# Kernel tuning notes

Measured on AMD Instinct MI355X. Metric: run time of the kernel, lower is better.

Reference implementation:

```python
import jax, jax.numpy as jnp
import numpy as np

B, S, D = 4, 2048, 256
H, RANK, DFF = 8, 8, 1024
DK = D // H
EPS = 1e-5


def _linear(x, W, b):
    # torch nn.Linear: y = x @ W.T + b, W shape (out, in)
    return jnp.einsum('bsd,od->bso', x, W) + b


def _layer_norm(x, g, b):
    mu = jnp.mean(x, axis=-1, keepdims=True)
    var = jnp.var(x, axis=-1, keepdims=True)
    return (x - mu) * jax.lax.rsqrt(var + EPS) * g + b


def setup_inputs() -> dict:
    key = jax.random.key(0)
    ks = jax.random.split(key, 20)
    r = RANK * H
    s = lambda fan_in: 1.0 / np.sqrt(fan_in)
    inp = {
        'x': jax.random.normal(ks[0], (B, S, D), jnp.float32),
        'Wq_down': jax.random.uniform(ks[1], (r, D), jnp.float32, -s(D), s(D)),
        'bq_down': jnp.zeros((r,), jnp.float32),
        'Wq_up': jax.random.uniform(ks[2], (D, r), jnp.float32, -s(r), s(r)),
        'bq_up': jnp.zeros((D,), jnp.float32),
        'Wk_down': jax.random.uniform(ks[3], (r, D), jnp.float32, -s(D), s(D)),
        'bk_down': jnp.zeros((r,), jnp.float32),
        'Wk_up': jax.random.uniform(ks[4], (D, r), jnp.float32, -s(r), s(r)),
        'bk_up': jnp.zeros((D,), jnp.float32),
        'Wv': jax.random.uniform(ks[5], (D, D), jnp.float32, -s(D), s(D)),
        'bv': jnp.zeros((D,), jnp.float32),
        'Wo': jax.random.uniform(ks[6], (D, D), jnp.float32, -s(D), s(D)),
        'bo': jnp.zeros((D,), jnp.float32),
        'ln_attn_g': jnp.ones((D,), jnp.float32),
        'ln_attn_b': jnp.zeros((D,), jnp.float32),
        'W_ff1': jax.random.uniform(ks[7], (DFF, D), jnp.float32, -s(D), s(D)),
        'b_ff1': jnp.zeros((DFF,), jnp.float32),
        'W_ff2': jax.random.uniform(ks[8], (D, DFF), jnp.float32, -s(DFF), s(DFF)),
        'b_ff2': jnp.zeros((D,), jnp.float32),
        'ln_blk_g': jnp.ones((D,), jnp.float32),
        'ln_blk_b': jnp.zeros((D,), jnp.float32),
    }
    return inp


def reference(x, Wq_down, bq_down, Wq_up, bq_up, Wk_down, bk_down, Wk_up, bk_up,
              Wv, bv, Wo, bo, ln_attn_g, ln_attn_b,
              W_ff1, b_ff1, W_ff2, b_ff2, ln_blk_g, ln_blk_b):
    # Low-rank Q/K: down-project to rank*H then up-project to D
    Q = _linear(_linear(x, Wq_down, bq_down), Wq_up, bq_up)
    K = _linear(_linear(x, Wk_down, bk_down), Wk_up, bk_up)
    V = _linear(x, Wv, bv)
    # (B,S,D) -> (B,H,S,DK)
    Q = Q.reshape(B, S, H, DK).transpose(0, 2, 1, 3)
    K = K.reshape(B, S, H, DK).transpose(0, 2, 1, 3)
    V = V.reshape(B, S, H, DK).transpose(0, 2, 1, 3)
    scale = 1.0 / np.sqrt(DK).astype(np.float32)
    scores = jnp.einsum('bhqd,bhkd->bhqk', Q, K) * scale
    attn = jax.nn.softmax(scores, axis=-1)
    context = jnp.einsum('bhqk,bhkd->bhqd', attn, V)
    context = context.transpose(0, 2, 1, 3).reshape(B, S, D)
    attn_out = _linear(context, Wo, bo)
    attn_out = _layer_norm(x + attn_out, ln_attn_g, ln_attn_b)
    # FFN: Linear -> GELU (exact erf, torch default) -> Linear
    h = jax.nn.gelu(_linear(attn_out, W_ff1, b_ff1), approximate=False)
    ff = _linear(h, W_ff2, b_ff2)
    return _layer_norm(attn_out + ff, ln_blk_g, ln_blk_b)
```

## Files before the change

### kernel.cpp

```cpp
#include <hip/hip_runtime.h>
#include <hip/hip_bf16.h>
#include <math.h>

#define NB 4
#define NS 2048
#define ND 256
#define NH 8
#define NDK 32
#define NDFF 1024
#define NROWS (NB * NS)
#define KC 4
#define KVB 64
#define KTILES (NS / KC / KVB)
#define QVLD 384

using short8 = __attribute__((ext_vector_type(8))) short;
using f32x4  = __attribute__((ext_vector_type(4))) float;

__device__ __forceinline__ unsigned short f2bf(float f) {
  union { float f; unsigned u; } v; v.f = f;
  unsigned r = v.u + 0x7fffu + ((v.u >> 16) & 1u);
  return (unsigned short)(r >> 16);
}
__device__ __forceinline__ float bf2f(unsigned short u) {
  union { unsigned u; float f; } v; v.u = ((unsigned)u) << 16;
  return v.f;
}
__device__ __forceinline__ unsigned cvt_pk_bf16(float lo, float hi) {
  unsigned r;
  asm("v_cvt_pk_bf16_f32 %0, %1, %2" : "=v"(r) : "v"(lo), "v"(hi));
  return r;
}
__device__ __forceinline__ void gl_lds16(const void* g, void* l) {
  __builtin_amdgcn_global_load_lds(
      (const __attribute__((address_space(1))) unsigned int*)g,
      (__attribute__((address_space(3))) unsigned int*)l, 16, 0, 0);
}

__global__ void cvt_batch(const float* s0, const float* s1, const float* s2,
                          const float* s3, const float* s4, const float* s5,
                          const float* s6, const float* s7, const float* s8,
                          unsigned short* d0, unsigned short* d1,
                          unsigned short* d2, unsigned short* d3,
                          unsigned short* d4, unsigned short* d5,
                          unsigned short* d6, unsigned short* d7,
                          unsigned short* d8,
                          int n0, int n1, int n2, int n3, int n4, int n5,
                          int n6, int n7, int n8) {
  const float* s; unsigned short* d; int n;
  switch (blockIdx.y) {
    case 0: s = s0; d = d0; n = n0; break;
    case 1: s = s1; d = d1; n = n1; break;
    case 2: s = s2; d = d2; n = n2; break;
    case 3: s = s3; d = d3; n = n3; break;
    case 4: s = s4; d = d4; n = n4; break;
    case 5: s = s5; d = d5; n = n5; break;
    case 6: s = s6; d = d6; n = n6; break;
    case 7: s = s7; d = d7; n = n7; break;
    default: s = s8; d = d8; n = n8; break;
  }
  for (int i = (blockIdx.x * 256 + threadIdx.x) * 4; i < n; i += 512 * 256 * 4) {
    float4 v = *reinterpret_cast<const float4*>(s + i);
    ushort4 o;
    o.x = f2bf(v.x); o.y = f2bf(v.y); o.z = f2bf(v.z); o.w = f2bf(v.w);
    *reinterpret_cast<ushort4*>(d + i) = o;
  }
}

template <int BM, int BN, int ACT, int OBF, int RES, int DUAL>
__global__ __launch_bounds__(256)
void gemm_nt(const unsigned short* __restrict__ A, int lda,
             const unsigned short* __restrict__ W,
             const float* __restrict__ bias, const float* __restrict__ bias2,
             int bsplit, const float* __restrict__ bias3, int bsplit2,
             const float* __restrict__ resid, void* __restrict__ outp,
             int K, int O,
             const unsigned short* A2, const unsigned short* W2,
             const float* biasB, void* outp2) {
  constexpr int MFW = BM / 32;
  constexpr int NFW = BN / 32;
  __shared__ __align__(16) unsigned short lA[2][BM * 64];
  __shared__ __align__(16) unsigned short lB[2][BN * 64];
  const int tid = threadIdx.x, lane = tid & 63, wid = tid >> 6;
  const int wr = wid >> 1, wc = wid & 1;
  const int l15 = lane & 15, lg = lane >> 4;
  const int bm = blockIdx.x, bn = blockIdx.y;

  const unsigned short* Ap = A;
  const unsigned short* Wp = W;
  const float* biasp = bias;
  void* outpp = outp;
  if (DUAL && blockIdx.z) { Ap = A2; Wp = W2; biasp = biasB; outpp = outp2; }

  auto stage = [&](int k0, int buf) {
#pragma unroll
    for (int it = 0; it < BM / 32; ++it) {
      int c = it * 256 + tid;
      int row = c >> 3, cc = (c & 7) ^ (row & 7);
      gl_lds16(Ap + (size_t)(bm * BM + row) * lda + k0 + cc * 8,
               &lA[buf][c * 8]);
    }
#pragma unroll
    for (int it = 0; it < BN / 32; ++it) {
      int c = it * 256 + tid;
      int row = c >> 3, cc = (c & 7) ^ (row & 7);
      gl_lds16(Wp + (size_t)(bn * BN + row) * K + k0 + cc * 8, &lB[buf][c * 8]);
    }
  };

  f32x4 acc[MFW][NFW];
#pragma unroll
  for (int i = 0; i < MFW; ++i)
#pragma unroll
    for (int j = 0; j < NFW; ++j) acc[i][j] = (f32x4)0.0f;

  const int T = K >> 6;
  stage(0, 0);
  __syncthreads();
  for (int t = 0; t < T; ++t) {
    const int cur = t & 1;
    if (t + 1 < T) stage((t + 1) << 6, cur ^ 1);
#pragma unroll
    for (int kk = 0; kk < 2; ++kk) {
      short8 a[MFW], b[NFW];
#pragma unroll
      for (int mf = 0; mf < MFW; ++mf) {
        int row = wr * (BM / 2) + mf * 16 + l15;
        a[mf] = *reinterpret_cast<const short8*>(
            &lA[cur][row * 64 + (((kk * 4 + lg) ^ (l15 & 7)) << 3)]);
      }
#pragma unroll
      for (int nf = 0; nf < NFW; ++nf) {
        int row = wc * (BN / 2) + nf * 16 + l15;
        b[nf] = *reinterpret_cast<const short8*>(
            &lB[cur][row * 64 + (((kk * 4 + lg) ^ (l15 & 7)) << 3)]);
      }
#pragma unroll
      for (int mf = 0; mf < MFW; ++mf)
#pragma unroll
        for (int nf = 0; nf < NFW; ++nf)
          acc[mf][nf] = __builtin_amdgcn_mfma_f32_16x16x32_bf16(
              a[mf], b[nf], acc[mf][nf], 0, 0, 0);
    }
    __syncthreads();
  }

#pragma unroll
  for (int mf = 0; mf < MFW; ++mf)
#pragma unroll
    for (int nf = 0; nf < NFW; ++nf) {
      int col = bn * BN + wc * (BN / 2) + nf * 16 + l15;
      float bv;
      if (bias3 && col >= bsplit2) bv = bias3[col - bsplit2];
      else if (bias2 && col >= bsplit) bv = bias2[col - bsplit];
      else bv = biasp[col];
#pragma unroll
      for (int i = 0; i < 4; ++i) {
        int row = bm * BM + wr * (BM / 2) + mf * 16 + lg * 4 + i;
        float v = acc[mf][nf][i] + bv;
        if (ACT == 1) v = 0.5f * v * (1.0f + erff(v * 0.70710678118654752f));
        if (RES) v += resid[(size_t)row * O + col];
        if (OBF)
          ((unsigned short*)outpp)[(size_t)row * O + col] = f2bf(v);
        else
          ((float*)outpp)[(size_t)row * O + col] = v;
      }
    }
}

__global__ __launch_bounds__(256)
void attn_kernel(const unsigned short* __restrict__ Qb,
                 const unsigned short* __restrict__ Kb,
                 const unsigned short* __restrict__ qv,
                 unsigned short* __restrict__ pacc,
                 float* __restrict__ pl) {
  __shared__ __align__(16) unsigned short lK[2][KVB * 32];
  __shared__ __align__(16) unsigned short lVt[2][32 * 72];
  __shared__ __align__(16) unsigned short lP[4][16 * 64];
  const int tid = threadIdx.x, lane = tid & 63, wid = tid >> 6;
  const int l15 = lane & 15, lg = lane >> 4;
  const int bh = blockIdx.x, qt = blockIdx.y, kc = blockIdx.z;
  const int b = bh >> 3, h = bh & 7;
  const size_t headoff = (size_t)h * NDK;
  const int qbase = qt * 128 + wid * 32;
  const int kv0 = kc * (NS / KC);
  const float qscale = 0.25508686f;

  short8 aq[2];
#pragma unroll
  for (int r = 0; r < 2; ++r) {
    short8 v = *reinterpret_cast<const short8*>(
        Qb + (size_t)(b * NS + qbase + r * 16 + l15) * ND + headoff + lg * 8);
#pragma unroll
    for (int j = 0; j < 8; ++j)
      v[j] = (short)f2bf(bf2f((unsigned short)v[j]) * qscale);
    aq[r] = v;
  }

  const int krow = tid >> 2;
  const unsigned short* kptr =
      Kb + (size_t)(b * NS + kv0 + krow) * ND + headoff +
      (((tid & 3) ^ ((tid >> 3) & 3)) << 3);
  const int vd0 = (tid & 15) * 2, vk0 = (tid >> 4) * 4;
  const unsigned short* vptr =
      qv + (size_t)(b * NS + kv0 + vk0) * QVLD + 128 + headoff + vd0;

  auto writeV = [&](const unsigned* w, int buf) {
    unsigned lo0 = (w[0] & 0xffffu) | (w[1] << 16);
    unsigned lo1 = (w[2] & 0xffffu) | (w[3] << 16);
    unsigned hi0 = (w[0] >> 16) | (w[1] & 0xffff0000u);
    unsigned hi1 = (w[2] >> 16) | (w[3] & 0xffff0000u);
    *reinterpret_cast<uint2*>(&lVt[buf][vd0 * 72 + vk0]) = make_uint2(lo0, lo1);
    *reinterpret_cast<uint2*>(&lVt[buf][(vd0 + 1) * 72 + vk0]) =
        make_uint2(hi0, hi1);
  };

  f32x4 accT[2][2];
#pragma unroll
  for (int r = 0; r < 2; ++r)
#pragma unroll
    for (int d = 0; d < 2; ++d) accT[r][d] = (f32x4)0.0f;
  float l[2] = {0.0f, 0.0f};

  unsigned vr[4];
  gl_lds16(kptr, &lK[0][tid * 8]);
#pragma unroll
  for (int u = 0; u < 4; ++u)
    vr[u] = *reinterpret_cast<const unsigned*>(vptr + (size_t)u * QVLD);
  writeV(vr, 0);
  __syncthreads();

  for (int kt = 0; kt < KTILES; ++kt) {
    const int cur = kt & 1, nxt = cur ^ 1;
    const bool pf = (kt + 1 < KTILES);
    if (pf) {
      kptr += (size_t)KVB * ND;
      vptr += (size_t)KVB * QVLD;
      gl_lds16(kptr, &lK[nxt][tid * 8]);
#pragma unroll
      for (int u = 0; u < 4; ++u)
        vr[u] = *reinterpret_cast<const unsigned*>(vptr + (size_t)u * QVLD);
    }

#pragma unroll
    for (int r = 0; r < 2; ++r) {
      f32x4 sT[4];
      __builtin_amdgcn_s_setprio(1);
#pragma unroll
      for (int t = 0; t < 4; ++t) {
        short8 bk = *reinterpret_cast<const short8*>(
            &lK[cur][(t * 16 + l15) * 32 +
                     ((lg ^ ((l15 >> 1) & 3)) << 3)]);
        sT[t] = __builtin_amdgcn_mfma_f32_16x16x32_bf16(
            bk, aq[r], (f32x4)0.0f, 0, 0, 0);
      }
      __builtin_amdgcn_s_setprio(0);
#pragma unroll
      for (int t = 0; t < 4; ++t) {
        float p0 = __builtin_amdgcn_exp2f(sT[t][0]);
        float p1 = __builtin_amdgcn_exp2f(sT[t][1]);
        float p2 = __builtin_amdgcn_exp2f(sT[t][2]);
        float p3 = __builtin_amdgcn_exp2f(sT[t][3]);
        l[r] += (p0 + p1) + (p2 + p3);
        unsigned w0 = cvt_pk_bf16(p0, p1);
        unsigned w1 = cvt_pk_bf16(p2, p3);
        int blk = (t << 1) | (lg >> 1);
        *reinterpret_cast<uint2*>(
            &lP[wid][l15 * 64 + ((blk ^ (l15 & 7)) << 3) + ((lg & 1) << 2)]) =
            make_uint2(w0, w1);
      }
      __builtin_amdgcn_s_setprio(1);
#pragma unroll
      for (int kk = 0; kk < 2; ++kk) {
        short8 pa = *reinterpret_cast<const short8*>(
            &lP[wid][l15 * 64 + (((kk * 4 + lg) ^ (l15 & 7)) << 3)]);
#pragma unroll
        for (int dt = 0; dt < 2; ++dt) {
          short8 bv = *reinterpret_cast<const short8*>(
              &lVt[cur][(dt * 16 + l15) * 72 + kk * 32 + lg * 8]);
          accT[r][dt] = __builtin_amdgcn_mfma_f32_16x16x32_bf16(
              bv, pa, accT[r][dt], 0, 0, 0);
        }
      }
      __builtin_amdgcn_s_setprio(0);
    }

    if (pf) writeV(vr, nxt);
    __syncthreads();
  }

#pragma unroll
  for (int r = 0; r < 2; ++r) {
    l[r] += __shfl_xor(l[r], 16);
    l[r] += __shfl_xor(l[r], 32);
  }

#pragma unroll
  for (int r = 0; r < 2; ++r) {
    int qg = qbase + r * 16 + l15;
    size_t rowbase = ((size_t)kc * 65536 + (size_t)bh * NS + qg) * 32;
#pragma unroll
    for (int dt = 0; dt < 2; ++dt) {
      unsigned w0 = cvt_pk_bf16(accT[r][dt][0], accT[r][dt][1]);
      unsigned w1 = cvt_pk_bf16(accT[r][dt][2], accT[r][dt][3]);
      *reinterpret_cast<uint2*>(&pacc[rowbase + dt * 16 + lg * 4]) =
          make_uint2(w0, w1);
    }
  }
  if (lane < 16) {
#pragma unroll
    for (int r = 0; r < 2; ++r) {
      int qg = qbase + r * 16 + l15;
      pl[(size_t)kc * 65536 + (size_t)bh * NS + qg] = l[r];
    }
  }
}

__global__ __launch_bounds__(256)
void attn_combine(const unsigned short* __restrict__ pacc,
                  const float* __restrict__ pl,
                  unsigned short* __restrict__ ctx) {
  int gid = blockIdx.x * 256 + threadIdx.x;
  int r = gid >> 2, d8 = (gid & 3) * 8;
  float L = 0.0f;
#pragma unroll
  for (int c = 0; c < KC; ++c) L += pl[(size_t)c * 65536 + r];
  float inv = 1.0f / L;
  float o[8];
#pragma unroll
  for (int j = 0; j < 8; ++j) o[j] = 0.0f;
#pragma unroll
  for (int c = 0; c < KC; ++c) {
    short8 a = *reinterpret_cast<const short8*>(
        &pacc[((size_t)c * 65536 + r) * 32 + d8]);
#pragma unroll
    for (int j = 0; j < 8; ++j) o[j] += bf2f((unsigned short)a[j]);
  }
  int bh = r >> 11, q = r & 2047;
  int b = bh >> 3, h = bh & 7;
  short8 out;
#pragma unroll
  for (int j = 0; j < 8; ++j) out[j] = (short)f2bf(o[j] * inv);
  *reinterpret_cast<short8*>(
      &ctx[((size_t)(b * NS + q)) * ND + h * 32 + d8]) = out;
}

__global__ __launch_bounds__(256)
void ln_res_kernel(const float* __restrict__ a,
                   const float* __restrict__ g, const float* __restrict__ be,
                   float* yf, unsigned short* yb) {
  int row = blockIdx.x * 4 + (threadIdx.x >> 6);
  int lane = threadIdx.x & 63;
  size_t off = (size_t)row * ND + lane * 4;
  float4 va = *reinterpret_cast<const float4*>(a + off);
  float v0 = va.x, v1 = va.y, v2 = va.z, v3 = va.w;
  float s = v0 + v1 + v2 + v3;
  float sq = v0 * v0 + v1 * v1 + v2 * v2 + v3 * v3;
#pragma unroll
  for (int o = 1; o < 64; o <<= 1) {
    s += __shfl_xor(s, o);
    sq += __shfl_xor(sq, o);
  }
  float mu = s * (1.0f / 256.0f);
  float var = sq * (1.0f / 256.0f) - mu * mu;
  float rs = rsqrtf(var + 1e-5f);
  float4 vg = *reinterpret_cast<const float4*>(g + lane * 4);
  float4 vbe = *reinterpret_cast<const float4*>(be + lane * 4);
  float o0 = (v0 - mu) * rs * vg.x + vbe.x;
  float o1 = (v1 - mu) * rs * vg.y + vbe.y;
  float o2 = (v2 - mu) * rs * vg.z + vbe.z;
  float o3 = (v3 - mu) * rs * vg.w + vbe.w;
  if (yf) *reinterpret_cast<float4*>(yf + off) = make_float4(o0, o1, o2, o3);
  if (yb) {
    ushort4 ob;
    ob.x = f2bf(o0); ob.y = f2bf(o1); ob.z = f2bf(o2); ob.w = f2bf(o3);
    *reinterpret_cast<ushort4*>(yb + off) = ob;
  }
}

extern "C" void kernel_launch(void* const* d_in, const int* in_sizes, int n_in,
                              void* d_out, int out_size, void* d_ws,
                              size_t ws_size, hipStream_t stream) {
  (void)in_sizes; (void)n_in; (void)out_size; (void)ws_size;
  const float* x   = (const float*)d_in[0];
  const float* Wqd = (const float*)d_in[1];
  const float* bqd = (const float*)d_in[2];
  const float* Wqu = (const float*)d_in[3];
  const float* bqu = (const float*)d_in[4];
  const float* Wkd = (const float*)d_in[5];
  const float* bkd = (const float*)d_in[6];
  const float* Wku = (const float*)d_in[7];
  const float* bku = (const float*)d_in[8];
  const float* Wv  = (const float*)d_in[9];
  const float* bv  = (const float*)d_in[10];
  const float* Wo  = (const float*)d_in[11];
  const float* bo  = (const float*)d_in[12];
  const float* g1  = (const float*)d_in[13];
  const float* be1 = (const float*)d_in[14];
  const float* Wf1 = (const float*)d_in[15];
  const float* bf1 = (const float*)d_in[16];
  const float* Wf2 = (const float*)d_in[17];
  const float* bf2 = (const float*)d_in[18];
  const float* g2  = (const float*)d_in[19];
  const float* be2 = (const float*)d_in[20];

  char* p = (char*)d_ws;
  auto alloc = [&](size_t bytes) {
    char* r = p;
    p += (bytes + 255) & ~(size_t)255;
    return r;
  };
  unsigned short* xb   = (unsigned short*)alloc((size_t)NROWS * ND * 2);
  unsigned short* wqkv = (unsigned short*)alloc(384 * 256 * 2);
  unsigned short* wqu  = (unsigned short*)alloc(256 * 64 * 2);
  unsigned short* wku  = (unsigned short*)alloc(256 * 64 * 2);
  unsigned short* wo   = (unsigned short*)alloc(256 * 256 * 2);
  unsigned short* wf1  = (unsigned short*)alloc(1024 * 256 * 2);
  unsigned short* wf2  = (unsigned short*)alloc(256 * 1024 * 2);
  unsigned short* qv   = (unsigned short*)alloc((size_t)NROWS * QVLD * 2);
  unsigned short* Qb   = (unsigned short*)alloc((size_t)NROWS * ND * 2);
  unsigned short* Kb   = (unsigned short*)alloc((size_t)NROWS * ND * 2);
  unsigned short* ctx  = (unsigned short*)alloc((size_t)NROWS * ND * 2);
  float*          y1   = (float*)alloc((size_t)NROWS * ND * 4);
  unsigned short* y1b  = (unsigned short*)alloc((size_t)NROWS * ND * 2);
  unsigned short* hb   = (unsigned short*)alloc((size_t)NROWS * NDFF * 2);
  float* ao = (float*)d_out;

  unsigned short* pacc = hb;
  float* pl = y1;

  cvt_batch<<<dim3(512, 9), 256, 0, stream>>>(
      x, Wqd, Wkd, Wqu, Wku, Wv, Wo, Wf1, Wf2,
      xb, wqkv, wqkv + 64 * 256, wqu, wku, wqkv + 128 * 256, wo, wf1, wf2,
      NROWS * ND, 64 * 256, 64 * 256, 256 * 64, 256 * 64, 256 * 256,
      256 * 256, 1024 * 256, 256 * 1024);

  gemm_nt<64, 64, 0, 1, 0, 0><<<dim3(128, 6), 256, 0, stream>>>(
      xb, 256, wqkv, bqd, bkd, 64, bv, 128, nullptr, qv, 256, QVLD,
      nullptr, nullptr, nullptr, nullptr);
  gemm_nt<64, 64, 0, 1, 0, 1><<<dim3(128, 4, 2), 256, 0, stream>>>(
      qv, QVLD, wqu, bqu, nullptr, 0, nullptr, 0, nullptr, Qb, 64, 256,
      qv + 64, wku, bku, Kb);

  attn_kernel<<<dim3(NB * NH, NS / 128, KC), 256, 0, stream>>>(
      Qb, Kb, qv, pacc, pl);
  attn_combine<<<dim3(1024), 256, 0, stream>>>(pacc, pl, ctx);

  gemm_nt<64, 64, 0, 0, 1, 0><<<dim3(128, 4), 256, 0, stream>>>(
      ctx, 256, wo, bo, nullptr, 0, nullptr, 0, x, ao, 256, 256,
      nullptr, nullptr, nullptr, nullptr);
  ln_res_kernel<<<NROWS / 4, 256, 0, stream>>>(ao, g1, be1, y1, y1b);

  gemm_nt<128, 128, 1, 1, 0, 0><<<dim3(64, 8), 256, 0, stream>>>(
      y1b, 256, wf1, bf1, nullptr, 0, nullptr, 0, nullptr, hb, 256, NDFF,
      nullptr, nullptr, nullptr, nullptr);
  gemm_nt<64, 64, 0, 0, 1, 0><<<dim3(128, 4), 256, 0, stream>>>(
      hb, 1024, wf2, bf2, nullptr, 0, nullptr, 0, y1, ao, 1024, 256,
      nullptr, nullptr, nullptr, nullptr);
  ln_res_kernel<<<NROWS / 4, 256, 0, stream>>>(ao, g2, be2,
                                               (float*)d_out, nullptr);
}
```

Measured before the change: 108.5 us.

## Fuse x fp32-to-bf16 conversion into QKV GEMM and batch attention row tiles

The separate conversion of x to bf16 is removed. The first projection GEMM now reads fp32 x directly, converts it to bf16 in registers and writes the result to LDS, which avoids a full write and re-read of a bf16 copy of x. The attention inner loop is reorganised so both query row tiles issue their QK MFMAs together, then do exp/pack, then PV, using a doubled per-wave P buffer in LDS. This gives the scheduler more independent work per phase, at the cost of more LDS use and more live registers, and the fused path uses synchronous global loads in place of direct global-to-LDS loads.

Measured after the change: 109.5 us. Within noise of the previous version (+0.9%).

```diff
diff --git a/kernel.cpp b/kernel.cpp
--- a/kernel.cpp
+++ b/kernel.cpp
@@ -39,14 +39,13 @@
 
 __global__ void cvt_batch(const float* s0, const float* s1, const float* s2,
                           const float* s3, const float* s4, const float* s5,
-                          const float* s6, const float* s7, const float* s8,
+                          const float* s6, const float* s7,
                           unsigned short* d0, unsigned short* d1,
                           unsigned short* d2, unsigned short* d3,
                           unsigned short* d4, unsigned short* d5,
                           unsigned short* d6, unsigned short* d7,
-                          unsigned short* d8,
                           int n0, int n1, int n2, int n3, int n4, int n5,
-                          int n6, int n7, int n8) {
+                          int n6, int n7) {
   const float* s; unsigned short* d; int n;
   switch (blockIdx.y) {
     case 0: s = s0; d = d0; n = n0; break;
@@ -56,10 +55,9 @@
     case 4: s = s4; d = d4; n = n4; break;
     case 5: s = s5; d = d5; n = n5; break;
     case 6: s = s6; d = d6; n = n6; break;
-    case 7: s = s7; d = d7; n = n7; break;
-    default: s = s8; d = d8; n = n8; break;
-  }
-  for (int i = (blockIdx.x * 256 + threadIdx.x) * 4; i < n; i += 512 * 256 * 4) {
+    default: s = s7; d = d7; n = n7; break;
+  }
+  for (int i = (blockIdx.x * 256 + threadIdx.x) * 4; i < n; i += 256 * 256 * 4) {
     float4 v = *reinterpret_cast<const float4*>(s + i);
     ushort4 o;
     o.x = f2bf(v.x); o.y = f2bf(v.y); o.z = f2bf(v.z); o.w = f2bf(v.w);
@@ -67,15 +65,15 @@
   }
 }
 
-template <int BM, int BN, int ACT, int OBF, int RES, int DUAL>
+template <int BM, int BN, int ACT, int OBF, int RES, int DUAL, int AF32>
 __global__ __launch_bounds__(256)
-void gemm_nt(const unsigned short* __restrict__ A, int lda,
+void gemm_nt(const void* __restrict__ Araw, int lda,
              const unsigned short* __restrict__ W,
              const float* __restrict__ bias, const float* __restrict__ bias2,
              int bsplit, const float* __restrict__ bias3, int bsplit2,
              const float* __restrict__ resid, void* __restrict__ outp,
              int K, int O,
-             const unsigned short* A2, const unsigned short* W2,
+             const void* A2, const unsigned short* W2,
              const float* biasB, void* outp2) {
   constexpr int MFW = BM / 32;
   constexpr int NFW = BN / 32;
@@ -86,7 +84,7 @@
   const int l15 = lane & 15, lg = lane >> 4;
   const int bm = blockIdx.x, bn = blockIdx.y;
 
-  const unsigned short* Ap = A;
+  const void* Ap = Araw;
   const unsigned short* Wp = W;
   const float* biasp = bias;
   void* outpp = outp;
@@ -97,8 +95,22 @@
     for (int it = 0; it < BM / 32; ++it) {
       int c = it * 256 + tid;
       int row = c >> 3, cc = (c & 7) ^ (row & 7);
-      gl_lds16(Ap + (size_t)(bm * BM + row) * lda + k0 + cc * 8,
-               &lA[buf][c * 8]);
+      if (AF32) {
+        const float* src =
+            (const float*)Ap + (size_t)(bm * BM + row) * lda + k0 + cc * 8;
+        float4 v0 = *reinterpret_cast<const float4*>(src);
+        float4 v1 = *reinterpret_cast<const float4*>(src + 4);
+        uint4 w;
+        w.x = cvt_pk_bf16(v0.x, v0.y);
+        w.y = cvt_pk_bf16(v0.z, v0.w);
+        w.z = cvt_pk_bf16(v1.x, v1.y);
+        w.w = cvt_pk_bf16(v1.z, v1.w);
+        *reinterpret_cast<uint4*>(&lA[buf][c * 8]) = w;
+      } else {
+        gl_lds16((const unsigned short*)Ap +
+                     (size_t)(bm * BM + row) * lda + k0 + cc * 8,
+                 &lA[buf][c * 8]);
+      }
     }
 #pragma unroll
     for (int it = 0; it < BN / 32; ++it) {
@@ -176,7 +188,7 @@
                  float* __restrict__ pl) {
   __shared__ __align__(16) unsigned short lK[2][KVB * 32];
   __shared__ __align__(16) unsigned short lVt[2][32 * 72];
-  __shared__ __align__(16) unsigned short lP[4][16 * 64];
+  __shared__ __align__(16) unsigned short lP[4][2][16 * 64];
   const int tid = threadIdx.x, lane = tid & 63, wid = tid >> 6;
   const int l15 = lane & 15, lg = lane >> 4;
   const int bh = blockIdx.x, qt = blockIdx.y, kc = blockIdx.z;
@@ -197,9 +209,8 @@
     aq[r] = v;
   }
 
-  const int krow = tid >> 2;
   const unsigned short* kptr =
-      Kb + (size_t)(b * NS + kv0 + krow) * ND + headoff +
+      Kb + (size_t)(b * NS + kv0 + (tid >> 2)) * ND + headoff +
       (((tid & 3) ^ ((tid >> 3) & 3)) << 3);
   const int vd0 = (tid & 15) * 2, vk0 = (tid >> 4) * 4;
   const unsigned short* vptr =
@@ -242,38 +253,43 @@
         vr[u] = *reinterpret_cast<const unsigned*>(vptr + (size_t)u * QVLD);
     }
 
-#pragma unroll
-    for (int r = 0; r < 2; ++r) {
-      f32x4 sT[4];
-      __builtin_amdgcn_s_setprio(1);
+    f32x4 sT[2][4];
+    __builtin_amdgcn_s_setprio(1);
+#pragma unroll
+    for (int r = 0; r < 2; ++r)
 #pragma unroll
       for (int t = 0; t < 4; ++t) {
         short8 bk = *reinterpret_cast<const short8*>(
-            &lK[cur][(t * 16 + l15) * 32 +
-                     ((lg ^ ((l15 >> 1) & 3)) << 3)]);
-        sT[t] = __builtin_amdgcn_mfma_f32_16x16x32_bf16(
+            &lK[cur][(t * 16 + l15) * 32 + ((lg ^ ((l15 >> 1) & 3)) << 3)]);
+        sT[r][t] = __builtin_amdgcn_mfma_f32_16x16x32_bf16(
             bk, aq[r], (f32x4)0.0f, 0, 0, 0);
       }
-      __builtin_amdgcn_s_setprio(0);
+    __builtin_amdgcn_s_setprio(0);
+
+#pragma unroll
+    for (int r = 0; r < 2; ++r)
 #pragma unroll
       for (int t = 0; t < 4; ++t) {
-        float p0 = __builtin_amdgcn_exp2f(sT[t][0]);
-        float p1 = __builtin_amdgcn_exp2f(sT[t][1]);
-        float p2 = __builtin_amdgcn_exp2f(sT[t][2]);
-        float p3 = __builtin_amdgcn_exp2f(sT[t][3]);
+        float p0 = __builtin_amdgcn_exp2f(sT[r][t][0]);
+        float p1 = __builtin_amdgcn_exp2f(sT[r][t][1]);
+        float p2 = __builtin_amdgcn_exp2f(sT[r][t][2]);
+        float p3 = __builtin_amdgcn_exp2f(sT[r][t][3]);
         l[r] += (p0 + p1) + (p2 + p3);
         unsigned w0 = cvt_pk_bf16(p0, p1);
         unsigned w1 = cvt_pk_bf16(p2, p3);
         int blk = (t << 1) | (lg >> 1);
         *reinterpret_cast<uint2*>(
-            &lP[wid][l15 * 64 + ((blk ^ (l15 & 7)) << 3) + ((lg & 1) << 2)]) =
-            make_uint2(w0, w1);
-      }
-      __builtin_amdgcn_s_setprio(1);
+            &lP[wid][r][l15 * 64 + ((blk ^ (l15 & 7)) << 3) +
+                        ((lg & 1) << 2)]) = make_uint2(w0, w1);
+      }
+
+    __builtin_amdgcn_s_setprio(1);
+#pragma unroll
+    for (int r = 0; r < 2; ++r)
 #pragma unroll
       for (int kk = 0; kk < 2; ++kk) {
         short8 pa = *reinterpret_cast<const short8*>(
-            &lP[wid][l15 * 64 + (((kk * 4 + lg) ^ (l15 & 7)) << 3)]);
+            &lP[wid][r][l15 * 64 + (((kk * 4 + lg) ^ (l15 & 7)) << 3)]);
 #pragma unroll
         for (int dt = 0; dt < 2; ++dt) {
           short8 bv = *reinterpret_cast<const short8*>(
@@ -282,8 +298,7 @@
               bv, pa, accT[r][dt], 0, 0, 0);
         }
       }
-      __builtin_amdgcn_s_setprio(0);
-    }
+    __builtin_amdgcn_s_setprio(0);
 
     if (pf) writeV(vr, nxt);
     __syncthreads();
@@ -410,7 +425,6 @@
     p += (bytes + 255) & ~(size_t)255;
     return r;
   };
-  unsigned short* xb   = (unsigned short*)alloc((size_t)NROWS * ND * 2);
   unsigned short* wqkv = (unsigned short*)alloc(384 * 256 * 2);
   unsigned short* wqu  = (unsigned short*)alloc(256 * 64 * 2);
   unsigned short* wku  = (unsigned short*)alloc(256 * 64 * 2);
@@ -429,16 +443,16 @@
   unsigned short* pacc = hb;
   float* pl = y1;
 
-  cvt_batch<<<dim3(512, 9), 256, 0, stream>>>(
-      x, Wqd, Wkd, Wqu, Wku, Wv, Wo, Wf1, Wf2,
-      xb, wqkv, wqkv + 64 * 256, wqu, wku, wqkv + 128 * 256, wo, wf1, wf2,
-      NROWS * ND, 64 * 256, 64 * 256, 256 * 64, 256 * 64, 256 * 256,
+  cvt_batch<<<dim3(256, 8), 256, 0, stream>>>(
+      Wqd, Wkd, Wqu, Wku, Wv, Wo, Wf1, Wf2,
+      wqkv, wqkv + 64 * 256, wqu, wku, wqkv + 128 * 256, wo, wf1, wf2,
+      64 * 256, 64 * 256, 256 * 64, 256 * 64, 256 * 256,
       256 * 256, 1024 * 256, 256 * 1024);
 
-  gemm_nt<64, 64, 0, 1, 0, 0><<<dim3(128, 6), 256, 0, stream>>>(
-      xb, 256, wqkv, bqd, bkd, 64, bv, 128, nullptr, qv, 256, QVLD,
+  gemm_nt<64, 64, 0, 1, 0, 0, 1><<<dim3(128, 6), 256, 0, stream>>>(
+      x, 256, wqkv, bqd, bkd, 64, bv, 128, nullptr, qv, 256, QVLD,
       nullptr, nullptr, nullptr, nullptr);
-  gemm_nt<64, 64, 0, 1, 0, 1><<<dim3(128, 4, 2), 256, 0, stream>>>(
+  gemm_nt<64, 64, 0, 1, 0, 1, 0><<<dim3(128, 4, 2), 256, 0, stream>>>(
       qv, QVLD, wqu, bqu, nullptr, 0, nullptr, 0, nullptr, Qb, 64, 256,
       qv + 64, wku, bku, Kb);
 
@@ -446,15 +460,15 @@
       Qb, Kb, qv, pacc, pl);
   attn_combine<<<dim3(1024), 256, 0, stream>>>(pacc, pl, ctx);
 
-  gemm_nt<64, 64, 0, 0, 1, 0><<<dim3(128, 4), 256, 0, stream>>>(
+  gemm_nt<64, 64, 0, 0, 1, 0, 0><<<dim3(128, 4), 256, 0, stream>>>(
       ctx, 256, wo, bo, nullptr, 0, nullptr, 0, x, ao, 256, 256,
       nullptr, nullptr, nullptr, nullptr);
   ln_res_kernel<<<NROWS / 4, 256, 0, stream>>>(ao, g1, be1, y1, y1b);
 
-  gemm_nt<128, 128, 1, 1, 0, 0><<<dim3(64, 8), 256, 0, stream>>>(
+  gemm_nt<128, 128, 1, 1, 0, 0, 0><<<dim3(64, 8), 256, 0, stream>>>(
       y1b, 256, wf1, bf1, nullptr, 0, nullptr, 0, nullptr, hb, 256, NDFF,
       nullptr, nullptr, nullptr, nullptr);
-  gemm_nt<64, 64, 0, 0, 1, 0><<<dim3(128, 4), 256, 0, stream>>>(
+  gemm_nt<64, 64, 0, 0, 1, 0, 0><<<dim3(128, 4), 256, 0, stream>>>(
       hb, 1024, wf2, bf2, nullptr, 0, nullptr, 0, y1, ao, 1024, 256,
       nullptr, nullptr, nullptr, nullptr);
   ln_res_kernel<<<NROWS / 4, 256, 0, stream>>>(ao, g2, be2,
```
